# Kernel optimization log

Hardware: AMD Instinct MI355X
Metric: run time of the kernel (lower is better)

The kernel has to match this reference:

```python
import jax, jax.numpy as jnp
import numpy as np

N = 20000       # nodes
E = 320000      # edges (before self-loops)
F_IN = 128
HID = 128
HEADS = 4
OUT_DIM = 2
B = 64          # graphs in batch
SLOPE = 0.2     # GATv2 leaky_relu negative slope (PyG default)


def _glorot(key, shape):
    fan_in, fan_out = shape[0], shape[1]
    limit = np.sqrt(6.0 / (fan_in + fan_out)).astype(np.float32)
    return jax.random.uniform(key, shape, jnp.float32, -limit, limit)


def setup_inputs() -> dict:
    key = jax.random.key(0)
    ks = jax.random.split(key, 24)
    inp = {
        'x': jax.random.normal(ks[0], (N, F_IN), jnp.float32),
        'edge_src': jax.random.randint(ks[1], (E,), 0, N),
        'edge_dst': jax.random.randint(ks[2], (E,), 0, N),
        'batch': jnp.sort(jax.random.randint(ks[3], (N,), 0, B)),
        # layer 1: in=F_IN, out=HEADS*HID, concat
        'Wl1': _glorot(ks[4], (F_IN, HEADS * HID)),
        'Wr1': _glorot(ks[5], (F_IN, HEADS * HID)),
        'bl1': jnp.zeros((HEADS * HID,), jnp.float32),
        'br1': jnp.zeros((HEADS * HID,), jnp.float32),
        'att1': _glorot(ks[6], (HEADS, HID)),
        'bias1': jnp.zeros((HEADS * HID,), jnp.float32),
        # layer 2: in=HEADS*HID, out=HEADS*HID, concat
        'Wl2': _glorot(ks[7], (HEADS * HID, HEADS * HID)),
        'Wr2': _glorot(ks[8], (HEADS * HID, HEADS * HID)),
        'bl2': jnp.zeros((HEADS * HID,), jnp.float32),
        'br2': jnp.zeros((HEADS * HID,), jnp.float32),
        'att2': _glorot(ks[9], (HEADS, HID)),
        'bias2': jnp.zeros((HEADS * HID,), jnp.float32),
        # layer 3: in=HEADS*HID, heads=1, concat=False -> out=HID
        'Wl3': _glorot(ks[10], (HEADS * HID, HID)),
        'Wr3': _glorot(ks[11], (HEADS * HID, HID)),
        'bl3': jnp.zeros((HID,), jnp.float32),
        'br3': jnp.zeros((HID,), jnp.float32),
        'att3': _glorot(ks[12], (1, HID)),
        'bias3': jnp.zeros((HID,), jnp.float32),
        # output MLP
        'W_mlp1': _glorot(ks[13], (HID, HID)),
        'b_mlp1': jnp.zeros((HID,), jnp.float32),
        'W_mlp2': _glorot(ks[14], (HID, OUT_DIM)),
        'b_mlp2': jnp.zeros((OUT_DIM,), jnp.float32),
    }
    return inp


def gatv2_layer(x, src, dst, Wl, Wr, bl, br, att, bias, concat):
    """PyG GATv2Conv (eval mode): alpha_ij = softmax_j over N(i) of a^T LeakyReLU(xl_j + xr_i)."""
    H, C = att.shape
    n = x.shape[0]
    xl = (x @ Wl + bl).reshape(n, H, C)   # source transform
    e = jax.nn.leaky_relu(xl[src] + (x @ Wr + br).reshape(n, H, C)[dst], SLOPE)  # [E,H,C]
    logits = jnp.einsum('ehc,hc->eh', e, att)                                    # [E,H]
    # segment softmax over destination node
    m = jax.ops.segment_max(logits, dst, num_segments=n)
    alpha = jnp.exp(logits - m[dst])
    denom = jax.ops.segment_sum(alpha, dst, num_segments=n)
    alpha = alpha / denom[dst]
    out = jax.ops.segment_sum(xl[src] * alpha[..., None], dst, num_segments=n)   # [N,H,C]
    out = out.reshape(n, H * C) if concat else out.mean(axis=1)
    return out + bias


def reference(x, edge_src, edge_dst, batch,
              Wl1, Wr1, bl1, br1, att1, bias1,
              Wl2, Wr2, bl2, br2, att2, bias2,
              Wl3, Wr3, bl3, br3, att3, bias3,
              W_mlp1, b_mlp1, W_mlp2, b_mlp2):
    n = x.shape[0]
    loop = jnp.arange(n, dtype=edge_src.dtype)
    src = jnp.concatenate([edge_src, loop])   # PyG add_self_loops=True
    dst = jnp.concatenate([edge_dst, loop])

    h = jax.nn.elu(gatv2_layer(x, src, dst, Wl1, Wr1, bl1, br1, att1, bias1, True))
    h = jax.nn.elu(gatv2_layer(h, src, dst, Wl2, Wr2, bl2, br2, att2, bias2, True))
    h = jax.nn.elu(gatv2_layer(h, src, dst, Wl3, Wr3, bl3, br3, att3, bias3, False))

    # global_mean_pool over graph ids
    counts = jnp.maximum(jax.ops.segment_sum(jnp.ones((n,), h.dtype), batch, num_segments=B), 1.0)
    pooled = jax.ops.segment_sum(h, batch, num_segments=B) / counts[:, None]

    hidden = jax.nn.relu(pooled @ W_mlp1 + b_mlp1)
    return hidden @ W_mlp2 + b_mlp2
```

## Files before the change

### kernel.cpp

```cpp
#include <hip/hip_runtime.h>
#include <math.h>


typedef __attribute__((ext_vector_type(4))) float f32x4;
typedef __attribute__((ext_vector_type(8))) _Float16 f16x8;
typedef __attribute__((ext_vector_type(4))) _Float16 f16x4;
typedef __attribute__((ext_vector_type(2))) _Float16 f16x2;

__device__ __forceinline__ float elu1(float x) {
    return (x > 0.f) ? x : (__expf(x) - 1.f);
}
__device__ __forceinline__ f16x2 pk_leaky(f16x2 s) {
    const f16x2 slope = {(_Float16)0.2f, (_Float16)0.2f};
    return __builtin_elementwise_max(s, s * slope);
}

__device__ __forceinline__ float dpp_sum16(float v) {
    int t;
    t = __builtin_amdgcn_mov_dpp(__float_as_int(v), 0xB1, 0xF, 0xF, true);
    v += __int_as_float(t);
    t = __builtin_amdgcn_mov_dpp(__float_as_int(v), 0x4E, 0xF, 0xF, true);
    v += __int_as_float(t);
    t = __builtin_amdgcn_mov_dpp(__float_as_int(v), 0x141, 0xF, 0xF, true);
    v += __int_as_float(t);
    t = __builtin_amdgcn_mov_dpp(__float_as_int(v), 0x140, 0xF, 0xF, true);
    v += __int_as_float(t);
    return v;
}

__global__ __launch_bounds__(256) void scan1_kernel(const int* __restrict__ cnt,
                                                    int* __restrict__ psum, int N) {
    __shared__ int red[256];
    int idx = blockIdx.x * 256 + threadIdx.x;
    red[threadIdx.x] = (idx < N) ? cnt[idx] : 0;
    __syncthreads();
    for (int s = 128; s > 0; s >>= 1) {
        if (threadIdx.x < s) red[threadIdx.x] += red[threadIdx.x + s];
        __syncthreads();
    }
    if (threadIdx.x == 0) psum[blockIdx.x] = red[0];
}
__global__ __launch_bounds__(128) void scan2_kernel(int* __restrict__ psum, int nch) {
    __shared__ int buf[128];
    int t = threadIdx.x;
    int v = (t < nch) ? psum[t] : 0;
    buf[t] = v;
    __syncthreads();
    for (int off = 1; off < 128; off <<= 1) {
        int x = (t >= off) ? buf[t - off] : 0;
        __syncthreads();
        buf[t] += x;
        __syncthreads();
    }
    if (t < nch) psum[t] = buf[t] - v;
}
__global__ __launch_bounds__(256) void scan3_kernel(const int* __restrict__ cnt,
                                                    const int* __restrict__ psum,
                                                    int* __restrict__ rowstart,
                                                    int* __restrict__ cursor, int N) {
    __shared__ int buf[256];
    int idx = blockIdx.x * 256 + threadIdx.x;
    int v = (idx < N) ? cnt[idx] : 0;
    buf[threadIdx.x] = v;
    __syncthreads();
    for (int off = 1; off < 256; off <<= 1) {
        int t = (threadIdx.x >= off) ? buf[threadIdx.x - off] : 0;
        __syncthreads();
        buf[threadIdx.x] += t;
        __syncthreads();
    }
    int excl = buf[threadIdx.x] - v + psum[blockIdx.x];
    if (idx < N) {
        rowstart[idx] = excl;
        cursor[idx]   = excl;
        if (idx == N - 1) rowstart[N] = excl + v;
    }
}

__global__ void scatter_kernel(const int* __restrict__ src, const int* __restrict__ dst,
                               int* __restrict__ cursor, int* __restrict__ csr_src,
                               int E, int N) {
    int e = blockIdx.x * 256 + threadIdx.x;
    if (e < E + N) {
        int d, s;
        if (e < E) { d = dst[e]; s = src[e]; }
        else       { d = e - E; s = e - E; }
        int pos = atomicAdd(&cursor[d], 1);
        csr_src[pos] = s;
    }
}

__device__ __forceinline__ void convWT_body(
    const float* __restrict__ Wl, const float* __restrict__ Wr,
    _Float16* __restrict__ Bth, _Float16* __restrict__ Btl,
    int K, int Nh, int bx, int by, int t) {
    __shared__ float tile[32][33];
    int kb = bx * 32;
    int nb = by * 32;
    int tx = t & 31;
    int ty = t >> 5;
#pragma unroll
    for (int j = 0; j < 4; ++j) {
        int kk = kb + ty + j * 8;
        int nn = nb + tx;
        float v = (nn < Nh) ? Wl[(size_t)kk * Nh + nn]
                            : Wr[(size_t)kk * Nh + (nn - Nh)];
        tile[ty + j * 8][tx] = v;
    }
    __syncthreads();
#pragma unroll
    for (int j = 0; j < 4; ++j) {
        int nn = nb + ty + j * 8;
        int kk = kb + tx;
        float v = tile[tx][ty + j * 8];
        _Float16 h = (_Float16)v;
        Bth[(size_t)nn * K + kk] = h;
        Btl[(size_t)nn * K + kk] = (_Float16)(v - (float)h);
    }
}

__global__ __launch_bounds__(256) void prep_kernel(
    const float* __restrict__ Wl1, const float* __restrict__ Wr1,
    _Float16* __restrict__ Wth1, _Float16* __restrict__ Wtl1,
    const float* __restrict__ Wl2, const float* __restrict__ Wr2,
    _Float16* __restrict__ Wth2, _Float16* __restrict__ Wtl2,
    const float* __restrict__ Wl3, const float* __restrict__ Wr3,
    _Float16* __restrict__ Wth3, _Float16* __restrict__ Wtl3,
    const float* __restrict__ X, _Float16* __restrict__ A,
    int n_valid, int n_total,
    const int* __restrict__ batch, int* __restrict__ gstart, int N, int B,
    const int* __restrict__ edst, int* __restrict__ cnt, int E) {
    int b = blockIdx.x;
    int t = threadIdx.x;
    if (b < 128) {
        convWT_body(Wl1, Wr1, Wth1, Wtl1, 128, 512, b & 3, b >> 2, t);
    } else if (b < 640) {
        int l = b - 128;
        convWT_body(Wl2, Wr2, Wth2, Wtl2, 512, 512, l & 15, l >> 4, t);
    } else if (b < 768) {
        int l = b - 640;
        convWT_body(Wl3, Wr3, Wth3, Wtl3, 512, 128, l & 15, l >> 4, t);
    } else if (b < 3328) {
        int i = ((b - 768) * 256 + t) * 4;
        if (i < n_total) {
            float4 v = (i < n_valid) ? *(const float4*)(X + i)
                                     : make_float4(0.f, 0.f, 0.f, 0.f);
            f16x4 h;
            h.x = (_Float16)v.x; h.y = (_Float16)v.y;
            h.z = (_Float16)v.z; h.w = (_Float16)v.w;
            *(f16x4*)(A + i) = h;
        }
    } else if (b < 3407) {
        int n = (b - 3328) * 256 + t;
        if (n > N) return;
        int cur  = (n < N) ? batch[n] : B;
        int prev = (n == 0) ? -1 : batch[n - 1];
        for (int g = prev + 1; g <= cur; ++g) gstart[g] = n;
    } else {
        int e = (b - 3407) * 256 + t;
        if (e < E + N) {
            int d = (e < E) ? edst[e] : (e - E);
            atomicAdd(&cnt[d], 1);
        }
    }
}

#define SCW 132
__global__ __launch_bounds__(256, 1) void gemm_f16_kernel(
    const _Float16* __restrict__ A,
    const _Float16* __restrict__ Bh, const _Float16* __restrict__ Bl,
    const float* __restrict__ biasL, const float* __restrict__ biasR, int Nh_,
    _Float16* __restrict__ P, _Float16* __restrict__ Q, int K, int NT) {
    __shared__ __align__(16) char smem[49152];
    float* sC = (float*)(smem);

    const int tid  = threadIdx.x;
    const int lane = tid & 63;
    const int wv   = tid >> 6;
    const int wm   = wv & 1;
    const int wn   = wv >> 1;
    const int fm   = lane & 15;
    const int q    = lane >> 4;
    const int qa   = q ^ ((fm >> 1) & 3);

    const int bi = blockIdx.x;
    const int kx = bi & 7;
    const int tt = bi >> 3;
    const int m0 = ((tt / NT) * 8 + kx) * 128;
    const int n0 = (tt % NT) * 128;

    const int r0  = lane >> 2;
    const int kcs = (((lane & 3) ^ ((lane >> 3) & 3)) << 3);

    f32x4 acc[4][4];
#pragma unroll
    for (int i = 0; i < 4; ++i)
#pragma unroll
        for (int j = 0; j < 4; ++j) {
            acc[i][j].x = 0.f; acc[i][j].y = 0.f;
            acc[i][j].z = 0.f; acc[i][j].w = 0.f;
        }

    const int nIters = K >> 5;
    int cur = 0;
    {
        char* base = smem;
#pragma unroll
        for (int j = 0; j < 2; ++j) {
            int wc  = wv * 2 + j;
            int row = wc * 16 + r0;
            size_t ga = (size_t)(m0 + row) * K + kcs;
            size_t gb = (size_t)(n0 + row) * K + kcs;
            int lofs = wc * 1024;
            __builtin_amdgcn_global_load_lds(
                (const __attribute__((address_space(1))) void*)(A + ga),
                (__attribute__((address_space(3))) void*)(base + lofs), 16, 0, 0);
            __builtin_amdgcn_global_load_lds(
                (const __attribute__((address_space(1))) void*)(Bh + gb),
                (__attribute__((address_space(3))) void*)(base + 8192 + lofs), 16, 0, 0);
            __builtin_amdgcn_global_load_lds(
                (const __attribute__((address_space(1))) void*)(Bl + gb),
                (__attribute__((address_space(3))) void*)(base + 16384 + lofs), 16, 0, 0);
        }
    }
    for (int it = 0; it < nIters; ++it) {
        __syncthreads();
        if (it + 1 < nIters) {
            char* base = smem + (cur ^ 1) * 24576;
            int ks = (it + 1) << 5;
#pragma unroll
            for (int j = 0; j < 2; ++j) {
                int wc  = wv * 2 + j;
                int row = wc * 16 + r0;
                size_t ga = (size_t)(m0 + row) * K + ks + kcs;
                size_t gb = (size_t)(n0 + row) * K + ks + kcs;
                int lofs = wc * 1024;
                __builtin_amdgcn_global_load_lds(
                    (const __attribute__((address_space(1))) void*)(A + ga),
                    (__attribute__((address_space(3))) void*)(base + lofs), 16, 0, 0);
                __builtin_amdgcn_global_load_lds(
                    (const __attribute__((address_space(1))) void*)(Bh + gb),
                    (__attribute__((address_space(3))) void*)(base + 8192 + lofs), 16, 0, 0);
                __builtin_amdgcn_global_load_lds(
                    (const __attribute__((address_space(1))) void*)(Bl + gb),
                    (__attribute__((address_space(3))) void*)(base + 16384 + lofs), 16, 0, 0);
            }
        }

        _Float16* cA  = (_Float16*)(smem + cur * 24576);
        _Float16* cBh = (_Float16*)(smem + cur * 24576 + 8192);
        _Float16* cBl = (_Float16*)(smem + cur * 24576 + 16384);
        f16x8 ah[4];
#pragma unroll
        for (int mi = 0; mi < 4; ++mi)
            ah[mi] = *(const f16x8*)&cA[(wm * 64 + mi * 16 + fm) * 32 + qa * 8];
#pragma unroll
        for (int ni = 0; ni < 4; ++ni) {
            int r = (wn * 64 + ni * 16 + fm) * 32 + qa * 8;
            f16x8 bh = *(const f16x8*)&cBh[r];
            f16x8 bl = *(const f16x8*)&cBl[r];
#pragma unroll
            for (int mi = 0; mi < 4; ++mi) {
                acc[mi][ni] = __builtin_amdgcn_mfma_f32_16x16x32_f16(ah[mi], bh, acc[mi][ni], 0, 0, 0);
                acc[mi][ni] = __builtin_amdgcn_mfma_f32_16x16x32_f16(ah[mi], bl, acc[mi][ni], 0, 0, 0);
            }
        }
        cur ^= 1;
    }

    float bsv[4];
#pragma unroll
    for (int ni = 0; ni < 4; ++ni) {
        int col = n0 + wn * 64 + ni * 16 + fm;
        bsv[ni] = (col < Nh_) ? biasL[col] : biasR[col - Nh_];
    }

    _Float16* dstbase = (n0 < Nh_) ? P : Q;
    const int col0 = (n0 < Nh_) ? n0 : (n0 - Nh_);

#pragma unroll
    for (int c = 0; c < 2; ++c) {
        __syncthreads();
        if (wm == c) {
#pragma unroll
            for (int mi = 0; mi < 4; ++mi)
#pragma unroll
                for (int ni = 0; ni < 4; ++ni) {
                    int base = (mi * 16 + q * 4) * SCW + wn * 64 + ni * 16 + fm;
                    sC[base]           = acc[mi][ni].x + bsv[ni];
                    sC[base + SCW]     = acc[mi][ni].y + bsv[ni];
                    sC[base + 2 * SCW] = acc[mi][ni].z + bsv[ni];
                    sC[base + 3 * SCW] = acc[mi][ni].w + bsv[ni];
                }
        }
        __syncthreads();
#pragma unroll
        for (int j = 0; j < 8; ++j) {
            int flat = j * 256 + tid;
            int row  = flat >> 5;
            int col  = (flat & 31) * 4;
            f32x4 v = *(const f32x4*)(sC + row * SCW + col);
            f16x4 hv;
            hv.x = (_Float16)v.x; hv.y = (_Float16)v.y;
            hv.z = (_Float16)v.z; hv.w = (_Float16)v.w;
            *(f16x4*)(dstbase + (size_t)(m0 + c * 64 + row) * Nh_ + col0 + col) = hv;
        }
    }
}


__device__ __forceinline__ void edge4_one(
    int s, const _Float16* __restrict__ P, int c0,
    const f16x2* r2, const f16x2* t2, float& l_run, float* acc) {
    union { f16x8 v; f16x2 p[4]; } h;
    h.v = *(const f16x8*)(P + ((size_t)s << 9) + c0);
    float p = 0.f;
#pragma unroll
    for (int k = 0; k < 4; ++k)
        p = __builtin_amdgcn_fdot2(pk_leaky(h.p[k] + r2[k]), t2[k], p, false);
    p = dpp_sum16(p);
    float w = __expf(p);
    l_run += w;
#pragma unroll
    for (int j = 0; j < 8; ++j)
        acc[j] = fmaf((float)h.v[j], w, acc[j]);
}

__global__ __launch_bounds__(128) void gat_edge4_kernel(
    const _Float16* __restrict__ P, const _Float16* __restrict__ Q,
    const float* __restrict__ att, const float* __restrict__ bias,
    const int* __restrict__ rowstart, const int* __restrict__ srcs,
    _Float16* __restrict__ H, int N) {
    int wv = threadIdx.x >> 6;
    int lane = threadIdx.x & 63;
    int n = blockIdx.x * 2 + wv;
    if (n >= N) return;
    int c0 = lane * 8;

    f16x8 rv = *(const f16x8*)(Q + (size_t)n * 512 + c0);
    f16x2 r2[4], t2[4];
#pragma unroll
    for (int k = 0; k < 4; ++k) {
        r2[k].x = rv[2 * k]; r2[k].y = rv[2 * k + 1];
        t2[k].x = (_Float16)att[c0 + 2 * k];
        t2[k].y = (_Float16)att[c0 + 2 * k + 1];
    }

    float acc[8];
#pragma unroll
    for (int j = 0; j < 8; ++j) acc[j] = 0.f;
    float l_run = 0.f;

    int beg = __builtin_amdgcn_readfirstlane(rowstart[n]);
    int end = __builtin_amdgcn_readfirstlane(rowstart[n + 1]);

    int i = beg;
    int s0 = srcs[i], s1 = srcs[i + 1], s2 = srcs[i + 2], s3 = srcs[i + 3];

    for (; i + 3 < end; ) {
        int f0 = srcs[i + 4], f1 = srcs[i + 5], f2 = srcs[i + 6], f3 = srcs[i + 7];
        int u0 = __builtin_amdgcn_readfirstlane(s0);
        int u1 = __builtin_amdgcn_readfirstlane(s1);
        int u2 = __builtin_amdgcn_readfirstlane(s2);
        int u3 = __builtin_amdgcn_readfirstlane(s3);
        union { f16x8 v; f16x2 p[4]; } h0, h1, h2, h3;
        h0.v = *(const f16x8*)(P + ((size_t)u0 << 9) + c0);
        h1.v = *(const f16x8*)(P + ((size_t)u1 << 9) + c0);
        h2.v = *(const f16x8*)(P + ((size_t)u2 << 9) + c0);
        h3.v = *(const f16x8*)(P + ((size_t)u3 << 9) + c0);
        float p0 = 0.f, p1 = 0.f, p2 = 0.f, p3 = 0.f;
#pragma unroll
        for (int k = 0; k < 4; ++k) {
            p0 = __builtin_amdgcn_fdot2(pk_leaky(h0.p[k] + r2[k]), t2[k], p0, false);
            p1 = __builtin_amdgcn_fdot2(pk_leaky(h1.p[k] + r2[k]), t2[k], p1, false);
            p2 = __builtin_amdgcn_fdot2(pk_leaky(h2.p[k] + r2[k]), t2[k], p2, false);
            p3 = __builtin_amdgcn_fdot2(pk_leaky(h3.p[k] + r2[k]), t2[k], p3, false);
        }
        p0 = dpp_sum16(p0);
        p1 = dpp_sum16(p1);
        p2 = dpp_sum16(p2);
        p3 = dpp_sum16(p3);
        float w0 = __expf(p0);
        float w1 = __expf(p1);
        float w2 = __expf(p2);
        float w3 = __expf(p3);
        l_run += (w0 + w1) + (w2 + w3);
#pragma unroll
        for (int j = 0; j < 8; ++j) {
            float a = fmaf((float)h0.v[j], w0, acc[j]);
            a = fmaf((float)h1.v[j], w1, a);
            a = fmaf((float)h2.v[j], w2, a);
            acc[j] = fmaf((float)h3.v[j], w3, a);
        }
        i += 4; s0 = f0; s1 = f1; s2 = f2; s3 = f3;
    }
    int rem = end - i;
    if (rem > 0) edge4_one(__builtin_amdgcn_readfirstlane(s0), P, c0, r2, t2, l_run, acc);
    if (rem > 1) edge4_one(__builtin_amdgcn_readfirstlane(s1), P, c0, r2, t2, l_run, acc);
    if (rem > 2) edge4_one(__builtin_amdgcn_readfirstlane(s2), P, c0, r2, t2, l_run, acc);

    float inv = 1.f / l_run;
    f16x8 oh;
#pragma unroll
    for (int j = 0; j < 8; ++j)
        oh[j] = (_Float16)elu1(acc[j] * inv + bias[c0 + j]);
    *(f16x8*)(H + (size_t)n * 512 + c0) = oh;
}

__global__ __launch_bounds__(128) void gat_edge1_kernel(
    const _Float16* __restrict__ P, const _Float16* __restrict__ Q,
    const float* __restrict__ att, const float* __restrict__ bias,
    const int* __restrict__ rowstart, const int* __restrict__ srcs,
    float* __restrict__ out, int N) {
    int wv = threadIdx.x >> 6;
    int lane = threadIdx.x & 63;
    int n = blockIdx.x * 2 + wv;
    if (n >= N) return;
    int qd = lane >> 4;
    int lq = lane & 15;
    int c0 = lq * 8;

    f16x8 rv = *(const f16x8*)(Q + (size_t)n * 128 + c0);
    f16x2 r2[4], t2[4];
#pragma unroll
    for (int k = 0; k < 4; ++k) {
        r2[k].x = rv[2 * k]; r2[k].y = rv[2 * k + 1];
        t2[k].x = (_Float16)att[c0 + 2 * k];
        t2[k].y = (_Float16)att[c0 + 2 * k + 1];
    }

    float acc[8];
#pragma unroll
    for (int j = 0; j < 8; ++j) acc[j] = 0.f;
    float l_run = 0.f;

    int beg = __builtin_amdgcn_readfirstlane(rowstart[n]);
    int end = __builtin_amdgcn_readfirstlane(rowstart[n + 1]);
    for (int e = beg + qd; e < end; e += 4) {
        int s = srcs[e];
        union { f16x8 v; f16x2 p[4]; } hv;
        hv.v = *(const f16x8*)(P + ((size_t)s << 7) + c0);
        float p = 0.f;
#pragma unroll
        for (int k = 0; k < 4; ++k)
            p = __builtin_amdgcn_fdot2(pk_leaky(hv.p[k] + r2[k]), t2[k], p, false);
        p = dpp_sum16(p);
        float w = __expf(p);
        l_run += w;
#pragma unroll
        for (int j = 0; j < 8; ++j)
            acc[j] = fmaf((float)hv.v[j], w, acc[j]);
    }
    l_run += __shfl_xor(l_run, 16, 64);
    l_run += __shfl_xor(l_run, 32, 64);
#pragma unroll
    for (int j = 0; j < 8; ++j) {
        acc[j] += __shfl_xor(acc[j], 16, 64);
        acc[j] += __shfl_xor(acc[j], 32, 64);
    }
    float inv = 1.f / l_run;
    int cw = c0 + qd * 2;
    float2 w2;
    w2.x = elu1(acc[qd * 2]     * inv + bias[cw]);
    w2.y = elu1(acc[qd * 2 + 1] * inv + bias[cw + 1]);
    *(float2*)(out + (size_t)n * 128 + cw) = w2;
}

__global__ __launch_bounds__(256) void poolmlp_kernel(
    const float* __restrict__ h3, const int* __restrict__ gstart,
    const float* __restrict__ W1, const float* __restrict__ b1,
    const float* __restrict__ W2, const float* __restrict__ b2,
    float* __restrict__ out) {
    __shared__ float red[256];
    __shared__ float pr[128];
    __shared__ float2 mred[128];
    int g = blockIdx.x;
    int t = threadIdx.x;
    int c = t & 127;
    int h = t >> 7;
    int gs = gstart[g], ge = gstart[g + 1];
    float s = 0.f;
    for (int n = gs + h; n < ge; n += 2) s += h3[(size_t)n * 128 + c];
    red[t] = s;
    __syncthreads();
    if (h == 0) {
        float tot = red[c] + red[c + 128];
        float cntf = fmaxf((float)(ge - gs), 1.f);
        pr[c] = tot / cntf;
    }
    __syncthreads();
    if (t < 128) {
        float hh = b1[t];
#pragma unroll 4
        for (int k = 0; k < 128; ++k) hh = fmaf(pr[k], W1[k * 128 + t], hh);
        hh = fmaxf(hh, 0.0f);
        mred[t] = make_float2(hh * W2[t * 2], hh * W2[t * 2 + 1]);
    }
    __syncthreads();
    for (int ss = 64; ss > 0; ss >>= 1) {
        if (t < ss) {
            mred[t].x += mred[t + ss].x;
            mred[t].y += mred[t + ss].y;
        }
        __syncthreads();
    }
    if (t == 0) {
        out[g * 2]     = mred[0].x + b2[0];
        out[g * 2 + 1] = mred[0].y + b2[1];
    }
}

extern "C" void kernel_launch(void* const* d_in, const int* in_sizes, int n_in,
                              void* d_out, int out_size, void* d_ws, size_t ws_size,
                              hipStream_t stream) {
    const float* x     = (const float*)d_in[0];
    const int*   esrc  = (const int*)d_in[1];
    const int*   edst  = (const int*)d_in[2];
    const int*   batch = (const int*)d_in[3];
    const float* Wl1   = (const float*)d_in[4];
    const float* Wr1   = (const float*)d_in[5];
    const float* bl1   = (const float*)d_in[6];
    const float* br1   = (const float*)d_in[7];
    const float* att1  = (const float*)d_in[8];
    const float* bias1 = (const float*)d_in[9];
    const float* Wl2   = (const float*)d_in[10];
    const float* Wr2   = (const float*)d_in[11];
    const float* bl2   = (const float*)d_in[12];
    const float* br2   = (const float*)d_in[13];
    const float* att2  = (const float*)d_in[14];
    const float* bias2 = (const float*)d_in[15];
    const float* Wl3   = (const float*)d_in[16];
    const float* Wr3   = (const float*)d_in[17];
    const float* bl3   = (const float*)d_in[18];
    const float* br3   = (const float*)d_in[19];
    const float* att3  = (const float*)d_in[20];
    const float* bias3 = (const float*)d_in[21];
    const float* Wm1   = (const float*)d_in[22];
    const float* bm1   = (const float*)d_in[23];
    const float* Wm2   = (const float*)d_in[24];
    const float* bm2   = (const float*)d_in[25];

    int N  = in_sizes[0] / 128;
    int E  = in_sizes[1];
    int ET = E + N;
    int B  = out_size / 2;
    const int Mp = 160 * 128;
    int nch = (N + 255) / 256;

    char* ws = (char*)d_ws;
    size_t off = 0;
    auto alloc = [&](size_t bytes) -> void* {
        void* p = ws + off;
        off += (bytes + 255) & ~(size_t)255;
        return p;
    };
    _Float16* P    = (_Float16*)alloc((size_t)Mp * 512 * 2);
    _Float16* Q    = (_Float16*)alloc((size_t)Mp * 512 * 2);
    _Float16* A1   = (_Float16*)alloc((size_t)Mp * 128 * 2);
    _Float16* Hb   = (_Float16*)alloc((size_t)Mp * 512 * 2);
    _Float16* Wth1 = (_Float16*)alloc((size_t)1024 * 128 * 2);
    _Float16* Wtl1 = (_Float16*)alloc((size_t)1024 * 128 * 2);
    _Float16* Wth2 = (_Float16*)alloc((size_t)1024 * 512 * 2);
    _Float16* Wtl2 = (_Float16*)alloc((size_t)1024 * 512 * 2);
    _Float16* Wth3 = (_Float16*)alloc((size_t)256 * 512 * 2);
    _Float16* Wtl3 = (_Float16*)alloc((size_t)256 * 512 * 2);
    float*    R3   = (float*)alloc((size_t)Mp * 128 * 4);
    int*    cnt      = (int*)alloc((size_t)N * 4);
    int*    psum     = (int*)alloc((size_t)(nch + 1) * 4);
    int*    rowstart = (int*)alloc((size_t)(N + 1) * 4);
    int*    cursor   = (int*)alloc((size_t)N * 4);
    int*    csr_src  = (int*)alloc((size_t)ET * 4 + 64);
    int*    gstart   = (int*)alloc((size_t)(B + 1) * 4);
    (void)ws_size;

    hipMemsetAsync(cnt, 0, (size_t)N * 4, stream);

    int cblocks = (ET + 255) / 256;
    prep_kernel<<<3407 + cblocks, 256, 0, stream>>>(
        Wl1, Wr1, Wth1, Wtl1, Wl2, Wr2, Wth2, Wtl2, Wl3, Wr3, Wth3, Wtl3,
        x, A1, N * 128, Mp * 128, batch, gstart, N, B, edst, cnt, E);

    scan1_kernel<<<nch, 256, 0, stream>>>(cnt, psum, N);
    scan2_kernel<<<1, 128, 0, stream>>>(psum, nch);
    scan3_kernel<<<nch, 256, 0, stream>>>(cnt, psum, rowstart, cursor, N);
    scatter_kernel<<<cblocks, 256, 0, stream>>>(esrc, edst, cursor, csr_src, E, N);

    int eblocks = (N + 1) / 2;

    gemm_f16_kernel<<<160 * 8, 256, 0, stream>>>(A1, Wth1, Wtl1, bl1, br1, 512, P, Q, 128, 8);
    gat_edge4_kernel<<<eblocks, 128, 0, stream>>>(P, Q, att1, bias1, rowstart, csr_src, Hb, N);

    gemm_f16_kernel<<<160 * 8, 256, 0, stream>>>(Hb, Wth2, Wtl2, bl2, br2, 512, P, Q, 512, 8);
    gat_edge4_kernel<<<eblocks, 128, 0, stream>>>(P, Q, att2, bias2, rowstart, csr_src, Hb, N);

    gemm_f16_kernel<<<160 * 2, 256, 0, stream>>>(Hb, Wth3, Wtl3, bl3, br3, 128, P, Q, 512, 2);
    gat_edge1_kernel<<<eblocks, 128, 0, stream>>>(P, Q, att3, bias3, rowstart, csr_src, R3, N);

    poolmlp_kernel<<<B, 256, 0, stream>>>(R3, gstart, Wm1, bm1, Wm2, bm2, (float*)d_out);
}
```

Measured before the change: 397.4 us.

## Load high-half B fragments directly into registers, bypassing LDS

The GEMM previously staged A, Bh and Bl tiles through double-buffered LDS. Now only A and Bl go through LDS, while each wave loads its Bh fragments straight from global memory into registers, double-buffered across a loop unrolled by two. This cuts LDS footprint and LDS read traffic, at the cost of uncoalesced per-lane global loads for Bh and more register pressure.

```diff
diff --git a/kernel.cpp b/kernel.cpp
--- a/kernel.cpp
+++ b/kernel.cpp
@@ -171,7 +171,7 @@
     const _Float16* __restrict__ Bh, const _Float16* __restrict__ Bl,
     const float* __restrict__ biasL, const float* __restrict__ biasR, int Nh_,
     _Float16* __restrict__ P, _Float16* __restrict__ Q, int K, int NT) {
-    __shared__ __align__(16) char smem[49152];
+    __shared__ __align__(16) char smem[34816];
     float* sC = (float*)(smem);
 
     const int tid  = threadIdx.x;
@@ -202,7 +202,8 @@
         }
 
     const int nIters = K >> 5;
-    int cur = 0;
+    const int brow = n0 + wn * 64 + fm;
+
     {
         char* base = smem;
 #pragma unroll
@@ -216,56 +217,104 @@
                 (const __attribute__((address_space(1))) void*)(A + ga),
                 (__attribute__((address_space(3))) void*)(base + lofs), 16, 0, 0);
             __builtin_amdgcn_global_load_lds(
-                (const __attribute__((address_space(1))) void*)(Bh + gb),
+                (const __attribute__((address_space(1))) void*)(Bl + gb),
                 (__attribute__((address_space(3))) void*)(base + 8192 + lofs), 16, 0, 0);
-            __builtin_amdgcn_global_load_lds(
-                (const __attribute__((address_space(1))) void*)(Bl + gb),
-                (__attribute__((address_space(3))) void*)(base + 16384 + lofs), 16, 0, 0);
-        }
-    }
-    for (int it = 0; it < nIters; ++it) {
+        }
+    }
+    f16x8 bhA0, bhA1, bhA2, bhA3, bhB0, bhB1, bhB2, bhB3;
+    bhA0 = *(const f16x8*)(Bh + (size_t)(brow)      * K + q * 8);
+    bhA1 = *(const f16x8*)(Bh + (size_t)(brow + 16) * K + q * 8);
+    bhA2 = *(const f16x8*)(Bh + (size_t)(brow + 32) * K + q * 8);
+    bhA3 = *(const f16x8*)(Bh + (size_t)(brow + 48) * K + q * 8);
+
+    int cur = 0;
+    for (int it = 0; it < nIters; it += 2) {
         __syncthreads();
         if (it + 1 < nIters) {
-            char* base = smem + (cur ^ 1) * 24576;
-            int ks = (it + 1) << 5;
+            char* base = smem + (cur ^ 1) * 16384;
+            int ks2 = (it + 1) << 5;
 #pragma unroll
             for (int j = 0; j < 2; ++j) {
                 int wc  = wv * 2 + j;
                 int row = wc * 16 + r0;
-                size_t ga = (size_t)(m0 + row) * K + ks + kcs;
-                size_t gb = (size_t)(n0 + row) * K + ks + kcs;
+                size_t ga = (size_t)(m0 + row) * K + ks2 + kcs;
+                size_t gb = (size_t)(n0 + row) * K + ks2 + kcs;
                 int lofs = wc * 1024;
                 __builtin_amdgcn_global_load_lds(
                     (const __attribute__((address_space(1))) void*)(A + ga),
                     (__attribute__((address_space(3))) void*)(base + lofs), 16, 0, 0);
                 __builtin_amdgcn_global_load_lds(
-                    (const __attribute__((address_space(1))) void*)(Bh + gb),
+                    (const __attribute__((address_space(1))) void*)(Bl + gb),
                     (__attribute__((address_space(3))) void*)(base + 8192 + lofs), 16, 0, 0);
+            }
+            bhB0 = *(const f16x8*)(Bh + (size_t)(brow)      * K + ks2 + q * 8);
+            bhB1 = *(const f16x8*)(Bh + (size_t)(brow + 16) * K + ks2 + q * 8);
+            bhB2 = *(const f16x8*)(Bh + (size_t)(brow + 32) * K + ks2 + q * 8);
+            bhB3 = *(const f16x8*)(Bh + (size_t)(brow + 48) * K + ks2 + q * 8);
+        }
+        {
+            _Float16* cA  = (_Float16*)(smem + cur * 16384);
+            _Float16* cBl = (_Float16*)(smem + cur * 16384 + 8192);
+            f16x8 ah[4];
+#pragma unroll
+            for (int mi = 0; mi < 4; ++mi)
+                ah[mi] = *(const f16x8*)&cA[(wm * 64 + mi * 16 + fm) * 32 + qa * 8];
+#pragma unroll
+            for (int ni = 0; ni < 4; ++ni) {
+                f16x8 bh = (ni == 0) ? bhA0 : (ni == 1) ? bhA1 : (ni == 2) ? bhA2 : bhA3;
+                f16x8 bl = *(const f16x8*)&cBl[(wn * 64 + ni * 16 + fm) * 32 + qa * 8];
+#pragma unroll
+                for (int mi = 0; mi < 4; ++mi) {
+                    acc[mi][ni] = __builtin_amdgcn_mfma_f32_16x16x32_f16(ah[mi], bh, acc[mi][ni], 0, 0, 0);
+                    acc[mi][ni] = __builtin_amdgcn_mfma_f32_16x16x32_f16(ah[mi], bl, acc[mi][ni], 0, 0, 0);
+                }
+            }
+            cur ^= 1;
+        }
+        if (it + 1 >= nIters) break;
+
+        __syncthreads();
+        if (it + 2 < nIters) {
+            char* base = smem + (cur ^ 1) * 16384;
+            int ks2 = (it + 2) << 5;
+#pragma unroll
+            for (int j = 0; j < 2; ++j) {
+                int wc  = wv * 2 + j;
+                int row = wc * 16 + r0;
+                size_t ga = (size_t)(m0 + row) * K + ks2 + kcs;
+                size_t gb = (size_t)(n0 + row) * K + ks2 + kcs;
+                int lofs = wc * 1024;
+                __builtin_amdgcn_global_load_lds(
+                    (const __attribute__((address_space(1))) void*)(A + ga),
+                    (__attribute__((address_space(3))) void*)(base + lofs), 16, 0, 0);
                 __builtin_amdgcn_global_load_lds(
                     (const __attribute__((address_space(1))) void*)(Bl + gb),
-                    (__attribute__((address_space(3))) void*)(base + 16384 + lofs), 16, 0, 0);
+                    (__attribute__((address_space(3))) void*)(base + 8192 + lofs), 16, 0, 0);
             }
-        }
-
-        _Float16* cA  = (_Float16*)(smem + cur * 24576);
-        _Float16* cBh = (_Float16*)(smem + cur * 24576 + 8192);
-        _Float16* cBl = (_Float16*)(smem + cur * 24576 + 16384);
-        f16x8 ah[4];
-#pragma unroll
-        for (int mi = 0; mi < 4; ++mi)
-            ah[mi] = *(const f16x8*)&cA[(wm * 64 + mi * 16 + fm) * 32 + qa * 8];
-#pragma unroll
-        for (int ni = 0; ni < 4; ++ni) {
-            int r = (wn * 64 + ni * 16 + fm) * 32 + qa * 8;
-            f16x8 bh = *(const f16x8*)&cBh[r];
-            f16x8 bl = *(const f16x8*)&cBl[r];
-#pragma unroll
-            for (int mi = 0; mi < 4; ++mi) {
-                acc[mi][ni] = __builtin_amdgcn_mfma_f32_16x16x32_f16(ah[mi], bh, acc[mi][ni], 0, 0, 0);
-                acc[mi][ni] = __builtin_amdgcn_mfma_f32_16x16x32_f16(ah[mi], bl, acc[mi][ni], 0, 0, 0);
+            bhA0 = *(const f16x8*)(Bh + (size_t)(brow)      * K + ks2 + q * 8);
+            bhA1 = *(const f16x8*)(Bh + (size_t)(brow + 16) * K + ks2 + q * 8);
+            bhA2 = *(const f16x8*)(Bh + (size_t)(brow + 32) * K + ks2 + q * 8);
+            bhA3 = *(const f16x8*)(Bh + (size_t)(brow + 48) * K + ks2 + q * 8);
+        }
+        {
+            _Float16* cA  = (_Float16*)(smem + cur * 16384);
+            _Float16* cBl = (_Float16*)(smem + cur * 16384 + 8192);
+            f16x8 ah[4];
+#pragma unroll
+            for (int mi = 0; mi < 4; ++mi)
+                ah[mi] = *(const f16x8*)&cA[(wm * 64 + mi * 16 + fm) * 32 + qa * 8];
+#pragma unroll
+            for (int ni = 0; ni < 4; ++ni) {
+                f16x8 bh = (ni == 0) ? bhB0 : (ni == 1) ? bhB1 : (ni == 2) ? bhB2 : bhB3;
+                f16x8 bl = *(const f16x8*)&cBl[(wn * 64 + ni * 16 + fm) * 32 + qa * 8];
+#pragma unroll
+                for (int mi = 0; mi < 4; ++mi) {
+                    acc[mi][ni] = __builtin_amdgcn_mfma_f32_16x16x32_f16(ah[mi], bh, acc[mi][ni], 0, 0, 0);
+                    acc[mi][ni] = __builtin_amdgcn_mfma_f32_16x16x32_f16(ah[mi], bl, acc[mi][ni], 0, 0, 0);
+                }
             }
-        }
-        cur ^= 1;
+            cur ^= 1;
+        }
     }
 
     float bsv[4];
```

New measurement: 461.5 us. +16.1%, slower.
